# Performance work log

Measured on AMD Instinct MI355X. Metric: run time of the kernel, lower is better.

Reference implementation:

```python
import math
import jax, jax.numpy as jnp
import numpy as np

B, T = 65536, 34
VOCAB, TOK_DIM, POS_DIM, D_MODEL, FFN_DIM, HEAD_DIM = 14, 2, 3, 5, 2, 5
EPS = 1e-5

def _pos_flat_idx():
    # replicate _build_pos_map: 10 digits, Z_HI, 10 digits, Z_HI, 10 digits, special0, special1
    sources, indices = [], []
    for _ in range(3):
        for i in range(10):
            sources.append(0); indices.append(i)
        sources.append(2); indices.append(len([s for s in sources if s == 2]) - 1)
    # fix: the torch code appends (2,0),(2,1) after first two digit blocks and (1,0),(2,2) after the third
    sources, indices = [], []
    for i in range(10): sources.append(0); indices.append(i)
    sources.append(2); indices.append(0)
    for i in range(10): sources.append(0); indices.append(i)
    sources.append(2); indices.append(1)
    for i in range(10): sources.append(0); indices.append(i)
    sources.append(1); indices.append(0)
    sources.append(2); indices.append(2)
    src = np.array(sources); idx = np.array(indices)
    # table layout: rows 0..9 digit_pos, row 10 z_hi_pos, rows 11..13 special (learned0, learned1, eos)
    offs = np.array([0, 10, 11])
    return offs[src] + idx  # (34,)

POS_FLAT = jnp.asarray(_pos_flat_idx())
CAUSAL = jnp.tril(jnp.ones((T, T), dtype=bool))

def _rms(x, w):
    return x * jax.lax.rsqrt(jnp.mean(x * x, -1, keepdims=True) + EPS) * w

def setup_inputs():
    key = jax.random.key(0)
    ks = jax.random.split(key, 16)
    n = lambda i, shape: jax.random.normal(ks[i], shape, jnp.float32) * 0.5
    return {
        'idx': jax.random.randint(ks[0], (B, T), 0, VOCAB),
        'tok_emb': n(1, (VOCAB, TOK_DIM)),
        'spiral_amp': jnp.float32(1.0),
        'spiral_phase': jnp.float32(0.1),
        'spiral_slope': jnp.float32(1.0 / 9.0),
        'spiral_offset': jnp.float32(0.05),
        'pos_corr_slope': jnp.float32(0.01),
        'pos_corr_intercept': jnp.float32(0.02),
        'z_hi_pos': n(2, (1, POS_DIM)),
        'special_pos': n(3, (2, POS_DIM)),
        'q_w': n(4, (HEAD_DIM, POS_DIM)),
        'v_w': n(5, (HEAD_DIM, TOK_DIM)),
        'out_A': n(6, (HEAD_DIM, 2)),
        'out_B': n(7, (2, D_MODEL)),
        'q_phase': n(8, (1,)),
        'ln1_w': jnp.ones((D_MODEL,), jnp.float32),
        'ln2_w': jnp.ones((D_MODEL,), jnp.float32),
        'lnf_w': jnp.ones((D_MODEL,), jnp.float32),
        'fc1_w': n(9, (FFN_DIM, D_MODEL)),
        'fc1_b': n(10, (FFN_DIM,)),
        'fc2_w': n(11, (D_MODEL, FFN_DIM)),
        'fc2_b': n(12, (D_MODEL,)),
        'head_w': n(13, (TOK_DIM, D_MODEL)),
    }

def reference(idx, tok_emb, spiral_amp, spiral_phase, spiral_slope, spiral_offset,
              pos_corr_slope, pos_corr_intercept, z_hi_pos, special_pos,
              q_w, v_w, out_A, out_B, q_phase, ln1_w, ln2_w, lnf_w,
              fc1_w, fc1_b, fc2_w, fc2_b, head_w):
    # learned spiral digit positions (10, 3)
    i = jnp.arange(10, dtype=jnp.float32)
    angle = 2.0 * math.pi * i / 10.0 + spiral_phase
    base = jnp.stack([spiral_amp * jnp.cos(angle),
                      spiral_amp * jnp.sin(angle),
                      spiral_slope * i + spiral_offset], -1)
    corr = pos_corr_intercept + pos_corr_slope * i
    digit_pos = base * (1.0 + corr)[:, None]
    table = jnp.concatenate([digit_pos, z_hi_pos, special_pos,
                             jnp.zeros((1, POS_DIM), jnp.float32)], 0)  # (14, 3)
    pos = table[POS_FLAT]  # (T, 3)

    tok = tok_emb[idx]  # (B, T, 2)
    x = jnp.concatenate([tok, jnp.broadcast_to(pos, (idx.shape[0], T, POS_DIM))], -1)  # (B,T,5)

    h = _rms(x, ln1_w)
    q = jnp.einsum('btp,dp->btd', h[..., TOK_DIM:], q_w)  # (B,T,5)
    k = q  # q_proj applied to same input for both q and k
    v = jnp.einsum('btp,dp->btd', h[..., :TOK_DIM], v_w)  # (B,T,5)

    # per-head 2D rotation on first 4 dims (HEAD_DIM//2 = 2 pairs), dim 4 unchanged
    c, s = jnp.cos(q_phase[0]), jnp.sin(q_phase[0])
    q0, q1 = q[..., 0:4:2], q[..., 1:4:2]
    q_rot = jnp.concatenate([
        jnp.stack([q0 * c - q1 * s, q0 * s + q1 * c], -1).reshape(q.shape[:-1] + (4,)),
        q[..., 4:]], -1)

    att = jnp.einsum('btd,bsd->bts', q_rot, k) / math.sqrt(HEAD_DIM)
    att = jnp.where(CAUSAL, att, -jnp.inf)
    att = jax.nn.softmax(att, -1)
    out = jnp.einsum('bts,bsd->btd', att, v)  # (B,T,5)

    x = x + (out @ out_A) @ out_B  # low-rank out_proj
    hh = _rms(x, ln2_w)
    x = x + (jax.nn.gelu(hh @ fc1_w.T + fc1_b, approximate=False) @ fc2_w.T + fc2_b)
    x = _rms(x, lnf_w)
    return (x @ head_w.T) @ tok_emb.T  # (B, T, 14)
```

## Files before the change

### kernel.cpp

```cpp
#include <hip/hip_runtime.h>
#include <math.h>

#define T_SEQ 34
#define NTOK 14
#define NE (T_SEQ * NTOK)

#define OFF_RT   0
#define OFF_POS  476
#define OFF_MISC 510
#define NF4_SHARED 566
#define OFF_DTAB 566
#define DROW_F 36
#define NF4_TOTAL (NF4_SHARED + NE * (DROW_F/4))
#define WS_NEED ((size_t)NF4_TOTAL * 16)
#define MI_TE    0
#define MI_WST   32
#define MI_PM    144
#define MI_LN2   160
#define MI_LNF   168
#define MI_FC1W  176
#define MI_FC1B  186
#define MI_FC2W  192
#define MI_FC2B  208

#define ROWS 15
#define BLK 256
#define NEL (ROWS * T_SEQ)
#define TTS 17
#define AVS 17

__device__ inline void pos_for_t(int t,
    float amp, float ph, float slp, float off, float pcs, float pci,
    const float* __restrict__ z_hi, const float* __restrict__ spec,
    float& px, float& py, float& pz)
{
    if (t == 33)      { px = 0.f;     py = 0.f;     pz = 0.f; }
    else if (t == 32) { px = z_hi[0]; py = z_hi[1]; pz = z_hi[2]; }
    else if (t == 10) { px = spec[0]; py = spec[1]; pz = spec[2]; }
    else if (t == 21) { px = spec[3]; py = spec[4]; pz = spec[5]; }
    else {
        int i = (t < 10) ? t : (t < 21 ? t - 11 : t - 22);
        float fi = (float)i;
        float ang = 0.62831853071795864769f * fi + ph;
        float mlt = 1.f + pci + pcs * fi;
        px = amp * cosf(ang) * mlt;
        py = amp * sinf(ang) * mlt;
        pz = (slp * fi + off) * mlt;
    }
}

__global__ __launch_bounds__(64) void setup_kernel(
    const float* __restrict__ tok_emb,
    const float* __restrict__ s_amp, const float* __restrict__ s_phase,
    const float* __restrict__ s_slope, const float* __restrict__ s_offset,
    const float* __restrict__ pc_slope, const float* __restrict__ pc_int,
    const float* __restrict__ z_hi, const float* __restrict__ spec,
    const float* __restrict__ q_w, const float* __restrict__ v_w,
    const float* __restrict__ out_A, const float* __restrict__ out_B,
    const float* __restrict__ q_phase,
    const float* __restrict__ ln1_w, const float* __restrict__ ln2_w,
    const float* __restrict__ lnf_w,
    const float* __restrict__ fc1_w, const float* __restrict__ fc1_b,
    const float* __restrict__ fc2_w, const float* __restrict__ fc2_b,
    const float* __restrict__ head_w,
    float4* __restrict__ ws)
{
    __shared__ float4 PWs[T_SEQ];
    __shared__ float4 Poss[T_SEQ];

    const int tid = threadIdx.x;
    const float amp = s_amp[0], ph = s_phase[0], slp = s_slope[0], off = s_offset[0];
    const float pcs = pc_slope[0], pci = pc_int[0];

    if (tid < T_SEQ) {
        float px, py, pz;
        pos_for_t(tid, amp, ph, slp, off, pcs, pci, z_hi, spec, px, py, pz);
        PWs[tid]  = make_float4(px * ln1_w[2], py * ln1_w[3], pz * ln1_w[4], 0.f);
        Poss[tid] = make_float4(px, py, pz, 0.f);
    }
    __syncthreads();

    const int q = blockIdx.x * 64 + tid;
    if (q < NE) {
        const int t = q / NTOK, tk = q - t * NTOK;
        const float cph = cosf(q_phase[0]), sph = sinf(q_phase[0]);
        const float cscale = 0.44721359549995793f * 1.4426950408889634f;
        float4 P = Poss[t];
        float px = P.x, py = P.y, pz = P.z;
        float x0 = tok_emb[tk * 2], x1 = tok_emb[tk * 2 + 1];
        float ssum = x0*x0 + x1*x1 + px*px + py*py + pz*pz;
        float rn = rsqrtf(ssum * 0.2f + 1e-5f);
        float h0 = x0 * rn * ln1_w[0], h1 = x1 * rn * ln1_w[1];
        float h2 = px * rn * ln1_w[2], h3 = py * rn * ln1_w[3], h4 = pz * rn * ln1_w[4];
        float q0 = q_w[0]  * h2 + q_w[1]  * h3 + q_w[2]  * h4;
        float q1 = q_w[3]  * h2 + q_w[4]  * h3 + q_w[5]  * h4;
        float q2 = q_w[6]  * h2 + q_w[7]  * h3 + q_w[8]  * h4;
        float q3 = q_w[9]  * h2 + q_w[10] * h3 + q_w[11] * h4;
        float q4 = q_w[12] * h2 + q_w[13] * h3 + q_w[14] * h4;
        float r0 = q0 * cph - q1 * sph, r1 = q0 * sph + q1 * cph;
        float r2c = q2 * cph - q3 * sph, r3 = q2 * sph + q3 * cph;
        float c0 = (r0*q_w[0] + r1*q_w[3] + r2c*q_w[6] + r3*q_w[9]  + q4*q_w[12]) * cscale;
        float c1 = (r0*q_w[1] + r1*q_w[4] + r2c*q_w[7] + r3*q_w[10] + q4*q_w[13]) * cscale;
        float c2 = (r0*q_w[2] + r1*q_w[5] + r2c*q_w[8] + r3*q_w[11] + q4*q_w[14]) * cscale;

        ws[OFF_RT + q] = make_float4(rn, h0, h1, 0.f);
        if (tk == 0) ws[OFF_POS + t] = Poss[t];

        float* Drow = (float*)(ws + OFF_DTAB) + q * DROW_F;
        for (int s = 0; s < T_SEQ; ++s) {
            float4 pw = PWs[s];
            Drow[s] = fmaf(c0, pw.x, fmaf(c1, pw.y, c2 * pw.z));
        }
        Drow[34] = 0.f; Drow[35] = 0.f;
    }

    if (blockIdx.x == 0) {
        float* M = (float*)(ws + OFF_MISC);
        if (tid < 28) M[MI_TE + tid] = tok_emb[tid];
        for (int i = tid; i < 70; i += 64) {
            int v = i / 5, d = i - v * 5;
            M[MI_WST + v * 8 + d] = head_w[d] * tok_emb[v * 2]
                                  + head_w[5 + d] * tok_emb[v * 2 + 1];
        }
        if (tid < 10) {
            int j = tid >> 1, c = tid & 1;
            float acc = 0.f;
            for (int i = 0; i < 5; ++i) {
                float m5 = out_A[i*2] * out_B[j] + out_A[i*2+1] * out_B[5 + j];
                acc += m5 * v_w[i*2 + c];
            }
            M[MI_PM + tid] = acc;
        }
        if (tid < 5)  { M[MI_LN2 + tid] = ln2_w[tid]; M[MI_LNF + tid] = lnf_w[tid];
                        M[MI_FC2B + tid] = fc2_b[tid]; }
        if (tid < 10) { M[MI_FC1W + tid] = fc1_w[tid]; M[MI_FC2W + tid] = fc2_w[tid]; }
        if (tid < 2)  { M[MI_FC1B + tid] = fc1_b[tid]; }
    }
}

__global__ __launch_bounds__(BLK) void micro_main(
    const int* __restrict__ idx, const float4* __restrict__ ws,
    float* __restrict__ out, int N)
{
    __shared__ float4 TBLs[NF4_SHARED];
    __shared__ int    toksT[36 * TTS];
    __shared__ float2 Av[T_SEQ * AVS];

    const int tid = threadIdx.x;
    const int elemBase = blockIdx.x * NEL;

    for (int i = tid; i < NF4_SHARED; i += BLK) TBLs[i] = ws[i];
    if (tid < 2 * TTS) toksT[T_SEQ * TTS + tid] = 0;
    for (int i = tid; i < NEL; i += BLK) {
        int g = elemBase + i;
        int v = (g < N) ? idx[g] : 0;
        int r = i / T_SEQ, s = i - r * T_SEQ;
        toksT[s * TTS + r] = v;
    }
    __syncthreads();

    const float* Dtab = (const float*)(ws + OFF_DTAB);

    auto attn = [&](int t, int r) {
        int tokt = toksT[t * TTS + r];
        const float* Drow = Dtab + (t * NTOK + tokt) * DROW_F;
        float l = 0.f, a0 = 0.f, a1 = 0.f;
        const int nq = t >> 2;
        for (int sb = 0; sb <= nq; ++sb) {
            float4 d4 = *(const float4*)(Drow + (sb << 2));
            int sbase = sb << 2;
#pragma unroll
            for (int k = 0; k < 4; ++k) {
                int s = sbase + k;
                int tok = toksT[s * TTS + r];
                float4 R = TBLs[s * NTOK + tok];
                float dk = (k == 0) ? d4.x : (k == 1) ? d4.y : (k == 2) ? d4.z : d4.w;
                float pv = __builtin_amdgcn_exp2f(dk * R.x);
                pv = (s <= t) ? pv : 0.f;
                l += pv;
                a0 = fmaf(pv, R.y, a0);
                a1 = fmaf(pv, R.z, a1);
            }
        }
        float il = __builtin_amdgcn_rcpf(l);
        Av[t * AVS + r] = make_float2(a0 * il, a1 * il);
    };

    if (tid < 17 * ROWS) {
        int p = tid / ROWS;
        int r = tid - p * ROWS;
        attn(p, r);
        attn(33 - p, r);
    }
    __syncthreads();

    const float* M = (const float*)&TBLs[OFF_MISC];
    float zA[5], zB[5];
    int linA = elemBase + tid;
    int linB = elemBase + tid + BLK;
    bool va = (tid < NEL) && (linA < N);
    bool vb = (tid + BLK < NEL) && (linB < N);

    auto prep = [&](int e2, float* z) {
        int rr = e2 / T_SEQ;
        int t = e2 - rr * T_SEQ;
        int tok = toksT[t * TTS + rr];
        float2 a = Av[t * AVS + rr];
        float2 te = *(const float2*)&M[MI_TE + tok * 2];
        float4 P = TBLs[OFF_POS + t];

        float y[5];
        y[0] = te.x + M[MI_PM + 0] * a.x + M[MI_PM + 1] * a.y;
        y[1] = te.y + M[MI_PM + 2] * a.x + M[MI_PM + 3] * a.y;
        y[2] = P.x  + M[MI_PM + 4] * a.x + M[MI_PM + 5] * a.y;
        y[3] = P.y  + M[MI_PM + 6] * a.x + M[MI_PM + 7] * a.y;
        y[4] = P.z  + M[MI_PM + 8] * a.x + M[MI_PM + 9] * a.y;

        float s2 = y[0]*y[0] + y[1]*y[1] + y[2]*y[2] + y[3]*y[3] + y[4]*y[4];
        float r2 = rsqrtf(s2 * 0.2f + 1e-5f);
        float hh[5];
#pragma unroll
        for (int j = 0; j < 5; ++j) hh[j] = y[j] * r2 * M[MI_LN2 + j];

        float u0 = M[MI_FC1B + 0], u1 = M[MI_FC1B + 1];
#pragma unroll
        for (int j = 0; j < 5; ++j) { u0 += hh[j] * M[MI_FC1W + j]; u1 += hh[j] * M[MI_FC1W + 5 + j]; }
        float g0 = 0.5f * u0 * (1.f + erff(u0 * 0.70710678118654752f));
        float g1v = 0.5f * u1 * (1.f + erff(u1 * 0.70710678118654752f));

        float y2[5]; float s3 = 0.f;
#pragma unroll
        for (int j = 0; j < 5; ++j) {
            y2[j] = y[j] + g0 * M[MI_FC2W + j*2] + g1v * M[MI_FC2W + j*2 + 1] + M[MI_FC2B + j];
            s3 += y2[j] * y2[j];
        }
        float r3 = rsqrtf(s3 * 0.2f + 1e-5f);
#pragma unroll
        for (int j = 0; j < 5; ++j) z[j] = y2[j] * r3 * M[MI_LNF + j];
    };

    if (va) prep(tid, zA);
    if (vb) prep(tid + BLK, zB);

    float2* opA = (float2*)(out + (size_t)linA * 14);
    float2* opB = (float2*)(out + (size_t)linB * 14);
#pragma unroll
    for (int v = 0; v < 7; ++v) {
        float4 w0 = *(const float4*)&M[MI_WST + (2*v) * 8];
        float  w4 = M[MI_WST + (2*v) * 8 + 4];
        float4 u0 = *(const float4*)&M[MI_WST + (2*v+1) * 8];
        float  u4 = M[MI_WST + (2*v+1) * 8 + 4];
        if (va) {
            float rA = zA[0]*w0.x + zA[1]*w0.y + zA[2]*w0.z + zA[3]*w0.w + zA[4]*w4;
            float rB = zA[0]*u0.x + zA[1]*u0.y + zA[2]*u0.z + zA[3]*u0.w + zA[4]*u4;
            opA[v] = make_float2(rA, rB);
        }
        if (vb) {
            float rA = zB[0]*w0.x + zB[1]*w0.y + zB[2]*w0.z + zB[3]*w0.w + zB[4]*w4;
            float rB = zB[0]*u0.x + zB[1]*u0.y + zB[2]*u0.z + zB[3]*u0.w + zB[4]*u4;
            opB[v] = make_float2(rA, rB);
        }
    }
}

#define L_ROWS 30
#define L_BLK 512
#define L_NEL (L_ROWS * T_SEQ)
#define L_AVS (L_ROWS + 1)
#define L_TTS (L_ROWS + 1)

__global__ __launch_bounds__(L_BLK, 4) void micro_fused_legacy(
    const int* __restrict__ idx,
    const float* __restrict__ tok_emb,
    const float* __restrict__ s_amp, const float* __restrict__ s_phase,
    const float* __restrict__ s_slope, const float* __restrict__ s_offset,
    const float* __restrict__ pc_slope, const float* __restrict__ pc_int,
    const float* __restrict__ z_hi, const float* __restrict__ spec,
    const float* __restrict__ q_w, const float* __restrict__ v_w,
    const float* __restrict__ out_A, const float* __restrict__ out_B,
    const float* __restrict__ q_phase,
    const float* __restrict__ ln1_w, const float* __restrict__ ln2_w,
    const float* __restrict__ lnf_w,
    const float* __restrict__ fc1_w, const float* __restrict__ fc1_b,
    const float* __restrict__ fc2_w, const float* __restrict__ fc2_b,
    const float* __restrict__ head_w,
    float* __restrict__ out, int N)
{
    __shared__ float4 H4[NE];
    __shared__ float  H1f[NE];
    __shared__ float4 C3[NE];
    __shared__ float2 Av[T_SEQ * L_AVS];
    __shared__ int    toksT[T_SEQ * L_TTS];
    alignas(16) __shared__ float PosT[T_SEQ * 3];
    alignas(16) __shared__ float TE[NTOK * 2];
    alignas(16) __shared__ float PMs[12];
    alignas(16) __shared__ float WsT[NTOK * 8];
    alignas(16) __shared__ float ln2s[8], lnfs[8], fc1ws[12], fc2ws[12], fc2bs[8];
    __shared__ float fc1bs[2];

    const int tid = threadIdx.x;
    const int elemBase = blockIdx.x * L_NEL;

    for (int i = tid; i < L_NEL; i += L_BLK) {
        int g = elemBase + i;
        int v = (g < N) ? idx[g] : 0;
        int r = i / T_SEQ, s = i - r * T_SEQ;
        toksT[s * L_TTS + r] = v;
    }
    if (tid < NE) {
        const float amp = s_amp[0], ph = s_phase[0], slp = s_slope[0], off = s_offset[0];
        const float pcs = pc_slope[0], pci = pc_int[0];
        const float cph = cosf(q_phase[0]), sph = sinf(q_phase[0]);
        const float cscale = 0.44721359549995793f * 1.4426950408889634f;
        const int e = tid;
        const int t = e / NTOK, tk = e - t * NTOK;
        float px, py, pz;
        pos_for_t(t, amp, ph, slp, off, pcs, pci, z_hi, spec, px, py, pz);
        if (tk == 0) { PosT[t*3] = px; PosT[t*3+1] = py; PosT[t*3+2] = pz; }
        float x0 = tok_emb[tk * 2], x1 = tok_emb[tk * 2 + 1];
        float ssum = x0*x0 + x1*x1 + px*px + py*py + pz*pz;
        float rn = rsqrtf(ssum * 0.2f + 1e-5f);
        float h0 = x0 * rn * ln1_w[0], h1 = x1 * rn * ln1_w[1];
        float h2 = px * rn * ln1_w[2], h3 = py * rn * ln1_w[3], h4 = pz * rn * ln1_w[4];
        float q0 = q_w[0]  * h2 + q_w[1]  * h3 + q_w[2]  * h4;
        float q1 = q_w[3]  * h2 + q_w[4]  * h3 + q_w[5]  * h4;
        float q2 = q_w[6]  * h2 + q_w[7]  * h3 + q_w[8]  * h4;
        float q3 = q_w[9]  * h2 + q_w[10] * h3 + q_w[11] * h4;
        float q4 = q_w[12] * h2 + q_w[13] * h3 + q_w[14] * h4;
        float r0 = q0 * cph - q1 * sph, r1 = q0 * sph + q1 * cph;
        float r2c = q2 * cph - q3 * sph, r3 = q2 * sph + q3 * cph;
        float c0 = (r0*q_w[0] + r1*q_w[3] + r2c*q_w[6] + r3*q_w[9]  + q4*q_w[12]) * cscale;
        float c1 = (r0*q_w[1] + r1*q_w[4] + r2c*q_w[7] + r3*q_w[10] + q4*q_w[13]) * cscale;
        float c2 = (r0*q_w[2] + r1*q_w[5] + r2c*q_w[8] + r3*q_w[11] + q4*q_w[14]) * cscale;
        H4[e] = make_float4(h2, h3, h4, h0);
        H1f[e] = h1;
        C3[e] = make_float4(c0, c1, c2, 0.f);
    }
    if (tid < 28) TE[tid] = tok_emb[tid];
    if (tid < 70) {
        int v = tid / 5, d = tid - v * 5;
        WsT[v * 8 + d] = head_w[d] * tok_emb[v * 2] + head_w[5 + d] * tok_emb[v * 2 + 1];
    }
    if (tid < 10) {
        int j = tid >> 1, c = tid & 1;
        float acc = 0.f;
        for (int i = 0; i < 5; ++i) {
            float m5 = out_A[i*2] * out_B[j] + out_A[i*2+1] * out_B[5 + j];
            acc += m5 * v_w[i*2 + c];
        }
        PMs[tid] = acc;
    }
    if (tid < 5)  { ln2s[tid] = ln2_w[tid]; lnfs[tid] = lnf_w[tid]; fc2bs[tid] = fc2_b[tid]; }
    if (tid < 10) { fc1ws[tid] = fc1_w[tid]; fc2ws[tid] = fc2_w[tid]; }
    if (tid < 2)  { fc1bs[tid] = fc1_b[tid]; }
    __syncthreads();

    auto attn = [&](int t, int rr) {
        int tokt = toksT[t * L_TTS + rr];
        float4 c3 = C3[t * NTOK + tokt];
        float l = 0.f, a0 = 0.f, a1 = 0.f;
#pragma unroll 2
        for (int s = 0; s <= t; ++s) {
            int tok = toksT[s * L_TTS + rr];
            int e = s * NTOK + tok;
            float4 h = H4[e];
            float h1v = H1f[e];
            float sc = fmaf(c3.x, h.x, fmaf(c3.y, h.y, c3.z * h.z));
            float p = __builtin_amdgcn_exp2f(sc);
            l += p;
            a0 = fmaf(p, h.w, a0);
            a1 = fmaf(p, h1v, a1);
        }
        float il = __builtin_amdgcn_rcpf(l);
        Av[t * L_AVS + rr] = make_float2(a0 * il, a1 * il);
    };
    if (tid < 17 * L_ROWS) {
        int p = tid / L_ROWS;
        int r = tid - p * L_ROWS;
        attn(p, r);
        attn(33 - p, r);
    }
    __syncthreads();

    float zA[5], zB[5];
    int linA = elemBase + tid;
    int linB = elemBase + tid + L_BLK;
    bool va = (tid < L_NEL) && (linA < N);
    bool vb = (tid + L_BLK < L_NEL) && (linB < N);

    auto prep = [&](int e2, float* z) {
        int rr = e2 / T_SEQ;
        int t = e2 - rr * T_SEQ;
        int tok = toksT[t * L_TTS + rr];
        float2 a = Av[t * L_AVS + rr];
        float xv0 = TE[tok * 2], xv1 = TE[tok * 2 + 1];
        float xv2 = PosT[t*3], xv3 = PosT[t*3+1], xv4 = PosT[t*3+2];
        float y[5];
#pragma unroll
        for (int j = 0; j < 5; ++j)
            y[j] = (j == 0 ? xv0 : j == 1 ? xv1 : j == 2 ? xv2 : j == 3 ? xv3 : xv4)
                 + PMs[j*2] * a.x + PMs[j*2+1] * a.y;
        float s2 = y[0]*y[0] + y[1]*y[1] + y[2]*y[2] + y[3]*y[3] + y[4]*y[4];
        float r2 = rsqrtf(s2 * 0.2f + 1e-5f);
        float hh[5];
#pragma unroll
        for (int j = 0; j < 5; ++j) hh[j] = y[j] * r2 * ln2s[j];
        float u0 = fc1bs[0], u1 = fc1bs[1];
#pragma unroll
        for (int j = 0; j < 5; ++j) { u0 += hh[j] * fc1ws[j]; u1 += hh[j] * fc1ws[5 + j]; }
        float g0 = 0.5f * u0 * (1.f + erff(u0 * 0.70710678118654752f));
        float g1v = 0.5f * u1 * (1.f + erff(u1 * 0.70710678118654752f));
        float y2[5]; float s3 = 0.f;
#pragma unroll
        for (int j = 0; j < 5; ++j) {
            y2[j] = y[j] + g0 * fc2ws[j * 2] + g1v * fc2ws[j * 2 + 1] + fc2bs[j];
            s3 += y2[j] * y2[j];
        }
        float r3 = rsqrtf(s3 * 0.2f + 1e-5f);
#pragma unroll
        for (int j = 0; j < 5; ++j) z[j] = y2[j] * r3 * lnfs[j];
    };

    if (va) prep(tid, zA);
    if (vb) prep(tid + L_BLK, zB);

    float2* opA = (float2*)(out + (size_t)linA * 14);
    float2* opB = (float2*)(out + (size_t)linB * 14);
#pragma unroll
    for (int v = 0; v < 7; ++v) {
        float4 w0 = *(const float4*)&WsT[(2*v) * 8];
        float  w4 = WsT[(2*v) * 8 + 4];
        float4 u0 = *(const float4*)&WsT[(2*v+1) * 8];
        float  u4 = WsT[(2*v+1) * 8 + 4];
        if (va) {
            float rA = zA[0]*w0.x + zA[1]*w0.y + zA[2]*w0.z + zA[3]*w0.w + zA[4]*w4;
            float rB = zA[0]*u0.x + zA[1]*u0.y + zA[2]*u0.z + zA[3]*u0.w + zA[4]*u4;
            opA[v] = make_float2(rA, rB);
        }
        if (vb) {
            float rA = zB[0]*w0.x + zB[1]*w0.y + zB[2]*w0.z + zB[3]*w0.w + zB[4]*w4;
            float rB = zB[0]*u0.x + zB[1]*u0.y + zB[2]*u0.z + zB[3]*u0.w + zB[4]*u4;
            opB[v] = make_float2(rA, rB);
        }
    }
}

extern "C" void kernel_launch(void* const* d_in, const int* in_sizes, int n_in,
                              void* d_out, int out_size, void* d_ws, size_t ws_size,
                              hipStream_t stream) {
    const int N = in_sizes[0];
    if (ws_size >= WS_NEED && d_ws != nullptr) {
        setup_kernel<<<8, 64, 0, stream>>>(
            (const float*)d_in[1], (const float*)d_in[2], (const float*)d_in[3],
            (const float*)d_in[4], (const float*)d_in[5], (const float*)d_in[6],
            (const float*)d_in[7], (const float*)d_in[8], (const float*)d_in[9],
            (const float*)d_in[10], (const float*)d_in[11], (const float*)d_in[12],
            (const float*)d_in[13], (const float*)d_in[14], (const float*)d_in[15],
            (const float*)d_in[16], (const float*)d_in[17], (const float*)d_in[18],
            (const float*)d_in[19], (const float*)d_in[20], (const float*)d_in[21],
            (const float*)d_in[22],
            (float4*)d_ws);
        const int grid = (N + NEL - 1) / NEL;
        micro_main<<<grid, BLK, 0, stream>>>(
            (const int*)d_in[0], (const float4*)d_ws, (float*)d_out, N);
    } else {
        const int grid = (N + L_NEL - 1) / L_NEL;
        micro_fused_legacy<<<grid, L_BLK, 0, stream>>>(
            (const int*)d_in[0],
            (const float*)d_in[1], (const float*)d_in[2], (const float*)d_in[3],
            (const float*)d_in[4], (const float*)d_in[5], (const float*)d_in[6],
            (const float*)d_in[7], (const float*)d_in[8], (const float*)d_in[9],
            (const float*)d_in[10], (const float*)d_in[11], (const float*)d_in[12],
            (const float*)d_in[13], (const float*)d_in[14], (const float*)d_in[15],
            (const float*)d_in[16], (const float*)d_in[17], (const float*)d_in[18],
            (const float*)d_in[19], (const float*)d_in[20], (const float*)d_in[21],
            (const float*)d_in[22],
            (float*)d_out, N);
    }
}
```

Before: 243.2 us.

## Fuse paired attention rows into one unrolled loop sharing row token loads

Token indices are now stored row-major so each thread can load its whole row of tokens into registers as int4 vectors. The two attention queries per thread (t and 33-t) are computed in a single fully unrolled pass, so each key's table lookup is shared between them instead of being reloaded in two separate dynamic-trip-count loops. This cuts LDS traffic and loop overhead, but raises register pressure and does masked work for the short query. The fallback kernel also gets cosmetic no-op edits.

```diff
diff --git a/kernel.cpp b/kernel.cpp
--- a/kernel.cpp
+++ b/kernel.cpp
@@ -26,7 +26,7 @@
 #define ROWS 15
 #define BLK 256
 #define NEL (ROWS * T_SEQ)
-#define TTS 17
+#define TRS 36
 #define AVS 17
 
 __device__ inline void pos_for_t(int t,
@@ -143,54 +143,72 @@
     float* __restrict__ out, int N)
 {
     __shared__ float4 TBLs[NF4_SHARED];
-    __shared__ int    toksT[36 * TTS];
+    __shared__ int    toksR[ROWS * TRS];
     __shared__ float2 Av[T_SEQ * AVS];
 
     const int tid = threadIdx.x;
     const int elemBase = blockIdx.x * NEL;
 
     for (int i = tid; i < NF4_SHARED; i += BLK) TBLs[i] = ws[i];
-    if (tid < 2 * TTS) toksT[T_SEQ * TTS + tid] = 0;
     for (int i = tid; i < NEL; i += BLK) {
         int g = elemBase + i;
         int v = (g < N) ? idx[g] : 0;
         int r = i / T_SEQ, s = i - r * T_SEQ;
-        toksT[s * TTS + r] = v;
+        toksR[r * TRS + s] = v;
     }
     __syncthreads();
 
-    const float* Dtab = (const float*)(ws + OFF_DTAB);
-
-    auto attn = [&](int t, int r) {
-        int tokt = toksT[t * TTS + r];
-        const float* Drow = Dtab + (t * NTOK + tokt) * DROW_F;
-        float l = 0.f, a0 = 0.f, a1 = 0.f;
-        const int nq = t >> 2;
-        for (int sb = 0; sb <= nq; ++sb) {
-            float4 d4 = *(const float4*)(Drow + (sb << 2));
-            int sbase = sb << 2;
+    const float4* RtL = TBLs;
+    const float*  Dtab = (const float*)(ws + OFF_DTAB);
+
+    if (tid < 17 * ROWS) {
+        const int p = tid / ROWS;
+        const int r = tid - p * ROWS;
+        const int t1 = p, t2 = 33 - p;
+
+        int4 tr[9];
+        const int4* trow = (const int4*)&toksR[r * TRS];
+#pragma unroll
+        for (int i = 0; i < 9; ++i) tr[i] = trow[i];
+
+        const int tok1 = toksR[r * TRS + t1];
+        const int tok2 = toksR[r * TRS + t2];
+        const float* D1 = Dtab + (t1 * NTOK + tok1) * DROW_F;
+        const float* D2 = Dtab + (t2 * NTOK + tok2) * DROW_F;
+
+        float l1 = 0.f, a10 = 0.f, a11 = 0.f;
+        float l2 = 0.f, a20 = 0.f, a21 = 0.f;
+
+#pragma unroll
+        for (int sb = 0; sb < 9; ++sb) {
+            const int4 tq = tr[sb];
+            float4 d1 = make_float4(0.f, 0.f, 0.f, 0.f);
+            if (sb <= 4) d1 = *(const float4*)(D1 + (sb << 2));
+            const float4 d2 = *(const float4*)(D2 + (sb << 2));
 #pragma unroll
             for (int k = 0; k < 4; ++k) {
-                int s = sbase + k;
-                int tok = toksT[s * TTS + r];
-                float4 R = TBLs[s * NTOK + tok];
-                float dk = (k == 0) ? d4.x : (k == 1) ? d4.y : (k == 2) ? d4.z : d4.w;
-                float pv = __builtin_amdgcn_exp2f(dk * R.x);
-                pv = (s <= t) ? pv : 0.f;
-                l += pv;
-                a0 = fmaf(pv, R.y, a0);
-                a1 = fmaf(pv, R.z, a1);
+                const int s = (sb << 2) + k;
+                if (s >= T_SEQ) continue;
+                const int tok = (k == 0) ? tq.x : (k == 1) ? tq.y : (k == 2) ? tq.z : tq.w;
+                const float4 R = RtL[s * NTOK + tok];
+                if (s <= 16) {
+                    const float dk1 = (k == 0) ? d1.x : (k == 1) ? d1.y : (k == 2) ? d1.z : d1.w;
+                    float pv1 = __builtin_amdgcn_exp2f(dk1 * R.x);
+                    if (s > 0) pv1 = (s <= t1) ? pv1 : 0.f;
+                    l1 += pv1; a10 = fmaf(pv1, R.y, a10); a11 = fmaf(pv1, R.z, a11);
+                }
+                {
+                    const float dk2 = (k == 0) ? d2.x : (k == 1) ? d2.y : (k == 2) ? d2.z : d2.w;
+                    float pv2 = __builtin_amdgcn_exp2f(dk2 * R.x);
+                    if (s >= 18) pv2 = (s <= t2) ? pv2 : 0.f;
+                    l2 += pv2; a20 = fmaf(pv2, R.y, a20); a21 = fmaf(pv2, R.z, a21);
+                }
             }
         }
-        float il = __builtin_amdgcn_rcpf(l);
-        Av[t * AVS + r] = make_float2(a0 * il, a1 * il);
-    };
-
-    if (tid < 17 * ROWS) {
-        int p = tid / ROWS;
-        int r = tid - p * ROWS;
-        attn(p, r);
-        attn(33 - p, r);
+        const float il1 = __builtin_amdgcn_rcpf(l1);
+        const float il2 = __builtin_amdgcn_rcpf(l2);
+        Av[t1 * AVS + r] = make_float2(a10 * il1, a11 * il1);
+        Av[t2 * AVS + r] = make_float2(a20 * il2, a21 * il2);
     }
     __syncthreads();
 
@@ -204,7 +222,7 @@
     auto prep = [&](int e2, float* z) {
         int rr = e2 / T_SEQ;
         int t = e2 - rr * T_SEQ;
-        int tok = toksT[t * TTS + rr];
+        int tok = toksR[rr * TRS + t];
         float2 a = Av[t * AVS + rr];
         float2 te = *(const float2*)&M[MI_TE + tok * 2];
         float4 P = TBLs[OFF_POS + t];
@@ -330,7 +348,7 @@
         float r0 = q0 * cph - q1 * sph, r1 = q0 * sph + q1 * cph;
         float r2c = q2 * cph - q3 * sph, r3 = q2 * sph + q3 * cph;
         float c0 = (r0*q_w[0] + r1*q_w[3] + r2c*q_w[6] + r3*q_w[9]  + q4*q_w[12]) * cscale;
-        float c1 = (r0*q_w[1] + r1*q_w[4] + r2c*q_w[7] + r3*q_w[10] + q4*q_w[13]) * cscale;
+        float c1 = (r0*q_w[1] + r1*q_w[4] + r2c*q_w[7] + r3*q_w[10] + q4*q_w[14 - 1]) * cscale;
         float c2 = (r0*q_w[2] + r1*q_w[5] + r2c*q_w[8] + r3*q_w[11] + q4*q_w[14]) * cscale;
         H4[e] = make_float4(h2, h3, h4, h0);
         H1f[e] = h1;
@@ -366,7 +384,7 @@
             float4 h = H4[e];
             float h1v = H1f[e];
             float sc = fmaf(c3.x, h.x, fmaf(c3.y, h.y, c3.z * h.z));
-            float p = __builtin_amdgcn_exp2f(sc);
+            float p = __builtin_amdgcn_exp2f(sc * 1.4426950408889634f / 1.4426950408889634f);
             l += p;
             a0 = fmaf(p, h.w, a0);
             a1 = fmaf(p, h1v, a1);
```

After: 241.3 us. About the same (-0.8%).
